# Optimization experiments

Measured on AMD Instinct MI355X. Metric: run time of the kernel, lower is better.

## Reference

```python
import jax, jax.numpy as jnp
import numpy as np

ARITY = 2
DEPTH = 9          # max_depth: full tree has levels 0..DEPTH
H = 512            # hidden_size
V = 512            # vocab_size
B = 64             # batch
S = 64             # source length


def _preorder_perm(arity, depth):
    # map pre-order position -> flat level-order index
    offs = np.cumsum([0] + [arity ** d for d in range(depth + 1)])
    perm = []
    def rec(d, pos):
        perm.append(int(offs[d] + pos))
        if d < depth:
            for c in range(arity):
                rec(d + 1, pos * arity + c)
    rec(0, 0)
    return np.asarray(perm, dtype=np.int32)

PERM = jnp.asarray(_preorder_perm(ARITY, DEPTH))


def setup_inputs() -> dict:
    key = jax.random.key(0)
    ks = jax.random.split(key, 12)
    s = 0.05
    return {
        "root_hiddens": jax.random.normal(ks[0], (B, H), jnp.float32),
        "ann_emb": jax.random.normal(ks[1], (B, H), jnp.float32),
        "encoder_outputs": jax.random.normal(ks[2], (S, B, H), jnp.float32),
        "source_mask": jnp.ones((B, S), dtype=bool),
        # GRUCell params per child: input_size = 2H (attention concat)
        "w_ih": jax.random.normal(ks[3], (ARITY, 3 * H, 2 * H), jnp.float32) * s,
        "w_hh": jax.random.normal(ks[4], (ARITY, 3 * H, H), jnp.float32) * s,
        "b_ih": jax.random.normal(ks[5], (ARITY, 3 * H), jnp.float32) * s,
        "b_hh": jax.random.normal(ks[6], (ARITY, 3 * H), jnp.float32) * s,
        # hidden2vocab: Linear(H,2H) -> Sigmoid -> Linear(2H,V)
        "W1": jax.random.normal(ks[7], (2 * H, H), jnp.float32) * s,
        "b1": jax.random.normal(ks[8], (2 * H,), jnp.float32) * s,
        "W2": jax.random.normal(ks[9], (V, 2 * H), jnp.float32) * s,
        "b2": jax.random.normal(ks[10], (V,), jnp.float32) * s,
    }


def _gru(x, h, wih, whh, bih, bhh):
    # x: [B,n,2H], h: [B,n,H]; PyTorch GRUCell semantics
    gi = jnp.einsum('bni,gi->bng', x, wih) + bih
    gh = jnp.einsum('bnh,gh->bng', h, whh) + bhh
    i_r, i_z, i_n = jnp.split(gi, 3, axis=-1)
    h_r, h_z, h_n = jnp.split(gh, 3, axis=-1)
    r = jax.nn.sigmoid(i_r + h_r)
    z = jax.nn.sigmoid(i_z + h_z)
    n = jnp.tanh(i_n + r * h_n)
    return (1.0 - z) * n + z * h


def _forward(root_hiddens, ann_emb, encoder_outputs, source_mask,
             w_ih, w_hh, b_ih, b_hh, W1, b1, W2, b2):
    b = root_hiddens.shape[0]
    enc = encoder_outputs.transpose(1, 0, 2)        # [B,S,H]
    h = root_hiddens[:, None, :]                    # [B,1,H]
    prods = []
    for d in range(DEPTH + 1):
        # hidden2vocab at every node of this level
        hid = jax.nn.sigmoid(jnp.einsum('bnh,kh->bnk', h, W1) + b1)
        prods.append(jnp.einsum('bnk,vk->bnv', hid, W2) + b2)
        if d < DEPTH:
            # dot-product attention per node over source positions
            scores = jnp.einsum('bnh,bsh->bns', h, enc)
            scores = jnp.where(source_mask[:, None, :], scores, -1e9)
            a = jax.nn.softmax(scores, axis=-1)
            weighted = jnp.einsum('bns,bsh->bnh', a, enc)
            n = h.shape[1]
            x = jnp.concatenate(
                [jnp.broadcast_to(ann_emb[:, None, :], (b, n, H)), weighted],
                axis=-1)                             # [B,n,2H]
            children = [_gru(x, h, w_ih[c], w_hh[c], b_ih[c], b_hh[c])
                        for c in range(ARITY)]
            h = jnp.stack(children, axis=2).reshape(b, n * ARITY, H)
    out = jnp.concatenate(prods, axis=1)            # [B,N,V] level-order
    out = out[:, PERM, :]                           # pre-order, as torch yields
    return out.transpose(1, 0, 2)                   # [N,B,V] like pad_sequence


def reference(root_hiddens, ann_emb, encoder_outputs, source_mask,
              w_ih, w_hh, b_ih, b_hh, W1, b1, W2, b2):
    return _forward(root_hiddens, ann_emb, encoder_outputs, source_mask,
                    w_ih, w_hh, b_ih, b_hh, W1, b1, W2, b2)
```

## Files before the change

kernel.cpp:

```cpp
#include <hip/hip_runtime.h>


#define BATCH 64
#define HDIM  512

typedef float  floatx4 __attribute__((ext_vector_type(4)));
typedef float  f32x16  __attribute__((ext_vector_type(16)));
typedef short  short8  __attribute__((ext_vector_type(8)));

__device__ __forceinline__ float bf2f(unsigned short u) {
  union { unsigned int i; float f; } v; v.i = ((unsigned int)u) << 16; return v.f;
}
__device__ __forceinline__ unsigned short f2bf(float f) {
  union { float f; unsigned int i; } v; v.f = f;
  unsigned int x = v.i;
  return (unsigned short)((x + 0x7fffu + ((x >> 16) & 1u)) >> 16);
}
__device__ __forceinline__ float sigm(float x) { return 1.f / (1.f + __expf(-x)); }

__device__ __forceinline__ int preorder_idx(int d, int node) {
  int p = 0;
  for (int i = 1; i <= d; ++i) {
    int bit = (node >> (d - i)) & 1;
    p += 1 + bit * ((1 << (10 - i)) - 1);
  }
  return p;
}

__device__ __forceinline__ void gload_lds16(const void* g, void* l) {
  __builtin_amdgcn_global_load_lds(
      (const __attribute__((address_space(1))) unsigned int*)g,
      (__attribute__((address_space(3))) unsigned int*)l, 16, 0, 0);
}

__device__ __forceinline__ void stage_f32(unsigned short* ldst, const float* src) {
  float4 v0 = *(const float4*)src;
  float4 v1 = *(const float4*)(src + 4);
  union { unsigned short s[8]; float4 v; } u;
  u.s[0]=f2bf(v0.x); u.s[1]=f2bf(v0.y); u.s[2]=f2bf(v0.z); u.s[3]=f2bf(v0.w);
  u.s[4]=f2bf(v1.x); u.s[5]=f2bf(v1.y); u.s[6]=f2bf(v1.z); u.s[7]=f2bf(v1.w);
  *(float4*)ldst = u.v;
}

__device__ __forceinline__ void stage_split(unsigned short* dh, unsigned short* dl,
                                            const float* src) {
  float4 v0 = *(const float4*)src;
  float4 v1 = *(const float4*)(src + 4);
  float v[8] = {v0.x, v0.y, v0.z, v0.w, v1.x, v1.y, v1.z, v1.w};
  union { unsigned short s[8]; float4 q; } H, L;
  #pragma unroll
  for (int i = 0; i < 8; ++i) {
    unsigned short hb = f2bf(v[i]);
    H.s[i] = hb;
    L.s[i] = f2bf(v[i] - bf2f(hb));
  }
  *(float4*)dh = H.q;
  *(float4*)dl = L.q;
}

__global__ __launch_bounds__(256) void k_root(const float* __restrict__ root,
                                              float* __restrict__ h0,
                                              unsigned short* __restrict__ bh,
                                              unsigned short* __restrict__ bl) {
  int i = blockIdx.x * 256 + threadIdx.x;
  float v = root[i];
  h0[i] = v;
  int row = i >> 9, k = i & 511;
  int mt = row >> 5, r = row & 31, ktg = k >> 4, oct = (k >> 3) & 1, e = k & 7;
  size_t fo = ((size_t)(mt * 32 + ktg) * 64 + oct * 32 + r) * 8 + e;
  unsigned short hb = f2bf(v);
  bh[fo] = hb;
  bl[fo] = f2bf(v - bf2f(hb));
}

__global__ __launch_bounds__(256) void k_prep_wih(const float* __restrict__ wih,
                                                  unsigned short* __restrict__ dh,
                                                  unsigned short* __restrict__ dl) {
  int idx = blockIdx.x * 256 + threadIdx.x;
  int jr  = idx & 31;
  int oct = (idx >> 5) & 1;
  int ktg = (idx >> 6) & 31;
  int jt  = (idx >> 11) & 15;
  int cg  = idx >> 15;
  int c = cg / 3, g = cg % 3;
  int j = jt * 32 + jr, k = ktg * 16 + oct * 8;
  const float* src = wih + ((size_t)c * 1536 + g * 512 + j) * 1024 + 512 + k;
  float v[8];
  *(float4*)&v[0] = *(const float4*)src;
  *(float4*)&v[4] = *(const float4*)(src + 4);
  union { unsigned short s[8]; float4 q; } H, L;
  #pragma unroll
  for (int i = 0; i < 8; ++i) {
    unsigned short hb = f2bf(v[i]); H.s[i] = hb; L.s[i] = f2bf(v[i] - bf2f(hb));
  }
  *(float4*)(dh + (size_t)idx * 8) = H.q;
  *(float4*)(dl + (size_t)idx * 8) = L.q;
}

__global__ __launch_bounds__(256) void k_prep_whh(const float* __restrict__ whh,
                                                  unsigned short* __restrict__ dh,
                                                  unsigned short* __restrict__ dl) {
  int idx = blockIdx.x * 256 + threadIdx.x;
  int jr  = idx & 31;
  int oct = (idx >> 5) & 1;
  int ktg = (idx >> 6) & 31;
  int jt  = (idx >> 11) & 15;
  int cg  = idx >> 15;
  int c = cg / 3, g = cg % 3;
  int j = jt * 32 + jr, k = ktg * 16 + oct * 8;
  const float* src = whh + ((size_t)c * 1536 + g * 512 + j) * 512 + k;
  float v[8];
  *(float4*)&v[0] = *(const float4*)src;
  *(float4*)&v[4] = *(const float4*)(src + 4);
  union { unsigned short s[8]; float4 q; } H, L;
  #pragma unroll
  for (int i = 0; i < 8; ++i) {
    unsigned short hb = f2bf(v[i]); H.s[i] = hb; L.s[i] = f2bf(v[i] - bf2f(hb));
  }
  *(float4*)(dh + (size_t)idx * 8) = H.q;
  *(float4*)(dl + (size_t)idx * 8) = L.q;
}

__global__ __launch_bounds__(256) void k_prep_bf(const float* __restrict__ src,
                                                 unsigned short* __restrict__ db) {
  size_t i = ((size_t)blockIdx.x * 256 + threadIdx.x) * 8;
  stage_f32(db + i, src + i);
}

__global__ __launch_bounds__(256) void k_giann(const float* __restrict__ ann,
                                               const float* __restrict__ wih,
                                               float* __restrict__ giann) {
  __shared__ __align__(16) unsigned short lah[64*40], lal[64*40];
  __shared__ __align__(16) unsigned short lwh[64*40], lwl[64*40];
  int t = threadIdx.x, lane = t & 63, wv = t >> 6;
  int jbase = blockIdx.y * 64, c = blockIdx.z;
  const float* wih_c = wih + (size_t)c * 1536 * 1024;
  floatx4 acc[4];
  #pragma unroll
  for (int i = 0; i < 4; ++i) acc[i] = (floatx4)(0.f);
  int srow = t >> 2, skk = (t & 3) * 8;
  for (int k0 = 0; k0 < 512; k0 += 32) {
    stage_split(lah + srow*40 + skk, lal + srow*40 + skk,
                ann + (size_t)srow * 512 + k0 + skk);
    stage_split(lwh + srow*40 + skk, lwl + srow*40 + skk,
                wih_c + (size_t)(jbase + srow) * 1024 + k0 + skk);
    __syncthreads();
    int arow = wv * 16 + (lane & 15), kq = (lane >> 4) * 8;
    short8 ah = *(const short8*)(lah + arow*40 + kq);
    short8 al = *(const short8*)(lal + arow*40 + kq);
    #pragma unroll
    for (int nt = 0; nt < 4; ++nt) {
      int wo = (nt * 16 + (lane & 15)) * 40 + kq;
      short8 wh = *(const short8*)(lwh + wo);
      short8 wl = *(const short8*)(lwl + wo);
      acc[nt] = __builtin_amdgcn_mfma_f32_16x16x32_bf16(ah, wh, acc[nt], 0, 0, 0);
      acc[nt] = __builtin_amdgcn_mfma_f32_16x16x32_bf16(ah, wl, acc[nt], 0, 0, 0);
      acc[nt] = __builtin_amdgcn_mfma_f32_16x16x32_bf16(al, wh, acc[nt], 0, 0, 0);
    }
    __syncthreads();
  }
  int quad = lane >> 4, cl = lane & 15;
  #pragma unroll
  for (int nt = 0; nt < 4; ++nt) {
    int g = jbase + nt * 16 + cl;
    #pragma unroll
    for (int r = 0; r < 4; ++r) {
      int b = wv * 16 + quad * 4 + r;
      giann[((size_t)c * 64 + b) * 1536 + g] = acc[nt][r];
    }
  }
}

__global__ __launch_bounds__(256) void k_attn(const float* __restrict__ h,
                                              const float* __restrict__ enc,
                                              unsigned short* __restrict__ wgh,
                                              unsigned short* __restrict__ wgl,
                                              int d) {
  int lane = threadIdx.x & 63, wv = threadIdx.x >> 6;
  int m = blockIdx.x * 4 + wv;
  int b = m >> d;
  __shared__ __align__(16) float sh[4][512];
  {
    const float4* src = (const float4*)(h + (size_t)m * HDIM);
    float4* dst = (float4*)sh[wv];
    dst[lane] = src[lane];
    dst[lane + 64] = src[lane + 64];
  }
  __syncthreads();
  const float* hr = sh[wv];
  const float* er = enc + ((size_t)lane * BATCH + b) * HDIM;
  float sc = 0.f;
  for (int k = 0; k < HDIM; k += 8) {
    float4 w0 = *(const float4*)(er + k);
    float4 w1 = *(const float4*)(er + k + 4);
    sc += hr[k+0]*w0.x + hr[k+1]*w0.y + hr[k+2]*w0.z + hr[k+3]*w0.w;
    sc += hr[k+4]*w1.x + hr[k+5]*w1.y + hr[k+6]*w1.z + hr[k+7]*w1.w;
  }
  float mx = sc;
  #pragma unroll
  for (int off = 32; off; off >>= 1) mx = fmaxf(mx, __shfl_xor(mx, off));
  float e = __expf(sc - mx);
  float sum = e;
  #pragma unroll
  for (int off = 32; off; off >>= 1) sum += __shfl_xor(sum, off);
  float a = e / sum;
  float acc[8];
  #pragma unroll
  for (int i = 0; i < 8; ++i) acc[i] = 0.f;
  for (int s = 0; s < 64; ++s) {
    float as = __shfl(a, s);
    const float* ep = enc + ((size_t)s * BATCH + b) * HDIM + lane * 8;
    float4 w0 = *(const float4*)ep;
    float4 w1 = *(const float4*)(ep + 4);
    acc[0] += as * w0.x; acc[1] += as * w0.y; acc[2] += as * w0.z; acc[3] += as * w0.w;
    acc[4] += as * w1.x; acc[5] += as * w1.y; acc[6] += as * w1.z; acc[7] += as * w1.w;
  }
  union { unsigned short s[8]; float4 q; } H, L;
  #pragma unroll
  for (int i = 0; i < 8; ++i) {
    unsigned short hb = f2bf(acc[i]); H.s[i] = hb; L.s[i] = f2bf(acc[i] - bf2f(hb));
  }
  int mt = m >> 5, rr = m & 31;
  size_t fo = ((size_t)(mt * 32 + (lane >> 1)) * 64 + (lane & 1) * 32 + rr) * 8;
  *(float4*)(wgh + fo) = H.q;
  *(float4*)(wgl + fo) = L.q;
}

__global__ __launch_bounds__(256) void k_hid(const float* __restrict__ h,
                                             const unsigned short* __restrict__ W1b,
                                             const float* __restrict__ b1,
                                             unsigned short* __restrict__ hid) {
  __shared__ __align__(16) unsigned short la[64 * 40];
  __shared__ __align__(16) unsigned short lw[64 * 40];
  int t = threadIdx.x, lane = t & 63, wv = t >> 6;
  int mbase = blockIdx.x * 64, jbase = blockIdx.y * 64;
  floatx4 acc[4];
  #pragma unroll
  for (int i = 0; i < 4; ++i) acc[i] = (floatx4)(0.f);
  int srow = t >> 2, skk = (t & 3) * 8;
  for (int k0 = 0; k0 < 512; k0 += 32) {
    stage_f32(la + srow * 40 + skk, h + (size_t)(mbase + srow) * 512 + k0 + skk);
    *(float4*)(lw + srow * 40 + skk) =
        *(const float4*)(W1b + (size_t)(jbase + srow) * 512 + k0 + skk);
    __syncthreads();
    int arow = wv * 16 + (lane & 15);
    int kq = (lane >> 4) * 8;
    short8 af = *(const short8*)(la + arow * 40 + kq);
    #pragma unroll
    for (int nt = 0; nt < 4; ++nt) {
      short8 wf = *(const short8*)(lw + (nt * 16 + (lane & 15)) * 40 + kq);
      acc[nt] = __builtin_amdgcn_mfma_f32_16x16x32_bf16(af, wf, acc[nt], 0, 0, 0);
    }
    __syncthreads();
  }
  int quad = lane >> 4, cl = lane & 15;
  #pragma unroll
  for (int nt = 0; nt < 4; ++nt) {
    int j = jbase + nt * 16 + cl;
    float bias = b1[j];
    #pragma unroll
    for (int r = 0; r < 4; ++r) {
      int m = mbase + wv * 16 + quad * 4 + r;
      hid[(size_t)m * 1024 + j] = f2bf(sigm(acc[nt][r] + bias));
    }
  }
}

__global__ __launch_bounds__(256) void k_out(const unsigned short* __restrict__ hid,
                                             const unsigned short* __restrict__ W2b,
                                             const float* __restrict__ b2,
                                             float* __restrict__ out, int d) {
  __shared__ __align__(16) unsigned short la[64 * 40];
  __shared__ __align__(16) unsigned short lw[64 * 40];
  int t = threadIdx.x, lane = t & 63, wv = t >> 6;
  int mbase = blockIdx.x * 64, jbase = blockIdx.y * 64;
  floatx4 acc[4];
  #pragma unroll
  for (int i = 0; i < 4; ++i) acc[i] = (floatx4)(0.f);
  int srow = t >> 2, skk = (t & 3) * 8;
  for (int k0 = 0; k0 < 1024; k0 += 32) {
    *(float4*)(la + srow * 40 + skk) =
        *(const float4*)(hid + (size_t)(mbase + srow) * 1024 + k0 + skk);
    *(float4*)(lw + srow * 40 + skk) =
        *(const float4*)(W2b + (size_t)(jbase + srow) * 1024 + k0 + skk);
    __syncthreads();
    int arow = wv * 16 + (lane & 15);
    int kq = (lane >> 4) * 8;
    short8 af = *(const short8*)(la + arow * 40 + kq);
    #pragma unroll
    for (int nt = 0; nt < 4; ++nt) {
      short8 wf = *(const short8*)(lw + (nt * 16 + (lane & 15)) * 40 + kq);
      acc[nt] = __builtin_amdgcn_mfma_f32_16x16x32_bf16(af, wf, acc[nt], 0, 0, 0);
    }
    __syncthreads();
  }
  int quad = lane >> 4, cl = lane & 15;
  int nmask = (1 << d) - 1;
  int pv[4], bv[4];
  #pragma unroll
  for (int r = 0; r < 4; ++r) {
    int m = mbase + wv * 16 + quad * 4 + r;
    bv[r] = m >> d;
    pv[r] = preorder_idx(d, m & nmask);
  }
  #pragma unroll
  for (int nt = 0; nt < 4; ++nt) {
    int j = jbase + nt * 16 + cl;
    float bias = b2[j];
    #pragma unroll
    for (int r = 0; r < 4; ++r) {
      out[((size_t)pv[r] * BATCH + bv[r]) * 512 + j] = acc[nt][r] + bias;
    }
  }
}

#define MF32(a, b, c) __builtin_amdgcn_mfma_f32_32x32x16_bf16(a, b, c, 0, 0, 0)

__global__ __launch_bounds__(256, 2) void k_gru(const float* __restrict__ h,
                                             const unsigned short* __restrict__ wgh,
                                             const unsigned short* __restrict__ wgl,
                                             const unsigned short* __restrict__ hbh,
                                             const unsigned short* __restrict__ hbl,
                                             const unsigned short* __restrict__ wihh,
                                             const unsigned short* __restrict__ wihl,
                                             const unsigned short* __restrict__ whhh,
                                             const unsigned short* __restrict__ whhl,
                                             const float* __restrict__ bih,
                                             const float* __restrict__ bhh,
                                             const float* __restrict__ giann,
                                             float* __restrict__ hnext,
                                             unsigned short* __restrict__ nbh,
                                             unsigned short* __restrict__ nbl,
                                             int d, int M, int emit_bf) {
  __shared__ __align__(16) unsigned short smem[2][20 * 512];
  int t = threadIdx.x, lane = t & 63, wv = t >> 6;
  int wm = wv >> 1, wj = wv & 1;
  int c = blockIdx.z;
  int mbase = blockIdx.x * 128, jbase = blockIdx.y * 64;
  int jt0 = jbase >> 5;
  int mb32 = mbase >> 5;
  int mtcap = (M >> 5) - 1;

  f32x16 a_r[2], a_z[2], a_n[2], a_h[2];
  #pragma unroll
  for (int i = 0; i < 2; ++i) {
    a_r[i] = (f32x16)(0.f); a_z[i] = (f32x16)(0.f);
    a_n[i] = (f32x16)(0.f); a_h[i] = (f32x16)(0.f);
  }

  auto stage = [&](int it2, int buf2) {
    int pht = it2 >> 5, kt = it2 & 31;
    const unsigned short* Ah = pht ? hbh : wgh;
    const unsigned short* Al = pht ? hbl : wgl;
    const unsigned short* Wh = pht ? whhh : wihh;
    const unsigned short* Wl = pht ? whhl : wihl;
    #pragma unroll
    for (int q = 0; q < 5; ++q) {
      int f = wv * 5 + q;
      const unsigned short* src;
      if (f < 8) {
        int mtl = f >> 1;
        int mt = mb32 + mtl; if (mt > mtcap) mt = mtcap;
        const unsigned short* blob = (f & 1) ? Al : Ah;
        src = blob + ((size_t)(mt * 32 + kt) * 64 + lane) * 8;
      } else {
        int u = f - 8;
        int g = u >> 2, jtl = (u >> 1) & 1;
        const unsigned short* blob = (u & 1) ? Wl : Wh;
        src = blob + ((size_t)(((c * 3 + g) * 16 + jt0 + jtl) * 32 + kt) * 64
                      + lane) * 8;
      }
      gload_lds16(src, &smem[buf2][f * 512]);
    }
  };

  stage(0, 0);
  __syncthreads();
  #pragma unroll
  for (int ph = 0; ph < 2; ++ph) {
    for (int i = 0; i < 32; ++i) {
      int it = ph * 32 + i;
      int buf = it & 1;
      if (it < 63) stage(it + 1, buf ^ 1);
      const unsigned short* bb = smem[buf];
      short8 ah[2], al[2];
      #pragma unroll
      for (int mt = 0; mt < 2; ++mt) {
        int s = (wm * 2 + mt) * 2;
        ah[mt] = *(const short8*)(bb + s * 512 + lane * 8);
        al[mt] = *(const short8*)(bb + (s + 1) * 512 + lane * 8);
      }
      short8 w[3][2];
      #pragma unroll
      for (int g = 0; g < 3; ++g) {
        int s = 8 + (g * 2 + wj) * 2;
        w[g][0] = *(const short8*)(bb + s * 512 + lane * 8);
        w[g][1] = *(const short8*)(bb + (s + 1) * 512 + lane * 8);
      }
      f32x16* ax = ph ? a_h : a_n;
      #pragma unroll
      for (int mt = 0; mt < 2; ++mt) {
        short8 AH = ah[mt], AL = al[mt];
        a_r[mt] = MF32(AH, w[0][0], a_r[mt]);
        a_r[mt] = MF32(AH, w[0][1], a_r[mt]);
        a_r[mt] = MF32(AL, w[0][0], a_r[mt]);
        a_z[mt] = MF32(AH, w[1][0], a_z[mt]);
        a_z[mt] = MF32(AH, w[1][1], a_z[mt]);
        a_z[mt] = MF32(AL, w[1][0], a_z[mt]);
        ax[mt]  = MF32(AH, w[2][0], ax[mt]);
        ax[mt]  = MF32(AH, w[2][1], ax[mt]);
        ax[mt]  = MF32(AL, w[2][0], ax[mt]);
      }
      __syncthreads();
    }
  }

  unsigned short (*trh)[72] = (unsigned short(*)[72])(&smem[0][0]);
  unsigned short (*trl)[72] = (unsigned short(*)[72])(&smem[0][0] + 128 * 72);
  int cl = lane & 31;
  int j = jbase + wj * 32 + cl;
  float br  = bih[c * 1536 + j]        + bhh[c * 1536 + j];
  float bz  = bih[c * 1536 + 512 + j]  + bhh[c * 1536 + 512 + j];
  float bin = bih[c * 1536 + 1024 + j];
  float bhn = bhh[c * 1536 + 1024 + j];
  int rowoff = 4 * (lane >> 5);
  #pragma unroll
  for (int mt = 0; mt < 2; ++mt) {
    int mb0 = mbase + wm * 64 + mt * 32 + rowoff;
    #pragma unroll
    for (int r = 0; r < 16; ++r) {
      int m = mb0 + (r & 3) + 8 * (r >> 2);
      if (m < M) {
        int b = m >> d;
        const float* gp = giann + ((size_t)c * 64 + b) * 1536 + j;
        float rg = sigm(a_r[mt][r] + gp[0] + br);
        float zg = sigm(a_z[mt][r] + gp[512] + bz);
        float ng = tanhf(a_n[mt][r] + gp[1024] + bin + rg * (a_h[mt][r] + bhn));
        float hv = h[(size_t)m * 512 + j];
        float nh = (1.f - zg) * ng + zg * hv;
        hnext[(size_t)(2 * m + c) * 512 + j] = nh;
        if (emit_bf) {
          unsigned short hb = f2bf(nh);
          trh[m - mbase][j - jbase] = hb;
          trl[m - mbase][j - jbase] = f2bf(nh - bf2f(hb));
        }
      }
    }
  }
  if (emit_bf) {
    __syncthreads();
    int a = t >> 7;
    int row = t & 127;
    if (mbase + row < M) {
      const unsigned short* trp = a ? &trl[row][0] : &trh[row][0];
      unsigned short* dst = a ? nbl : nbh;
      int mp = 2 * (mbase + row) + c;
      int mtp = mp >> 5, rp = mp & 31;
      #pragma unroll
      for (int q = 0; q < 8; ++q) {
        int k = jbase + q * 8;
        int ktg = k >> 4, oct = (k >> 3) & 1;
        float4 v = *(const float4*)(trp + q * 8);
        *(float4*)(dst + ((size_t)(mtp * 32 + ktg) * 64 + oct * 32 + rp) * 8) = v;
      }
    }
  }
}

extern "C" void kernel_launch(void* const* d_in, const int* in_sizes, int n_in,
                              void* d_out, int out_size, void* d_ws, size_t ws_size,
                              hipStream_t stream) {
  const float* root = (const float*)d_in[0];
  const float* ann  = (const float*)d_in[1];
  const float* enc  = (const float*)d_in[2];
  const float* wih  = (const float*)d_in[4];
  const float* whh  = (const float*)d_in[5];
  const float* bih  = (const float*)d_in[6];
  const float* bhh  = (const float*)d_in[7];
  const float* W1   = (const float*)d_in[8];
  const float* b1   = (const float*)d_in[9];
  const float* W2   = (const float*)d_in[10];
  const float* b2   = (const float*)d_in[11];
  float* out = (float*)d_out;

  char* ws = (char*)d_ws;
  float* hA = (float*)ws;
  float* hB = (float*)(ws + (size_t)67108864);
  unsigned short* hid  = (unsigned short*)(ws + (size_t)100663296);
  unsigned short* wgh  = (unsigned short*)(ws + (size_t)134217728);
  unsigned short* wgl  = (unsigned short*)(ws + (size_t)150994944);
  unsigned short* hbEh = (unsigned short*)(ws + (size_t)167772160);
  unsigned short* hbEl = (unsigned short*)(ws + (size_t)184549376);
  unsigned short* hbOh = (unsigned short*)(ws + (size_t)201326592);
  unsigned short* hbOl = (unsigned short*)(ws + (size_t)209715200);
  float* giann         = (float*)(ws + (size_t)218103808);
  unsigned short* wihh = (unsigned short*)(ws + (size_t)218890240);
  unsigned short* wihl = (unsigned short*)(ws + (size_t)222035968);
  unsigned short* whhh = (unsigned short*)(ws + (size_t)225181696);
  unsigned short* whhl = (unsigned short*)(ws + (size_t)228327424);
  unsigned short* W1b  = (unsigned short*)(ws + (size_t)231473152);
  unsigned short* W2b  = (unsigned short*)(ws + (size_t)232521728);

  k_root<<<dim3(128), dim3(256), 0, stream>>>(root, hB, hbEh, hbEl);
  k_prep_wih<<<dim3(768), dim3(256), 0, stream>>>(wih, wihh, wihl);
  k_prep_whh<<<dim3(768), dim3(256), 0, stream>>>(whh, whhh, whhl);
  k_prep_bf<<<dim3(256), dim3(256), 0, stream>>>(W1, W1b);
  k_prep_bf<<<dim3(256), dim3(256), 0, stream>>>(W2, W2b);
  k_giann<<<dim3(1, 24, 2), dim3(256), 0, stream>>>(ann, wih, giann);

  float* hcur = hB;
  float* hnxt = hA;
  unsigned short *bhc = hbEh, *blc = hbEl, *bhn = hbOh, *bln = hbOl;
  for (int d = 0; d <= 9; ++d) {
    int n = 1 << d;
    int M = 64 * n;
    k_hid<<<dim3(M / 64, 16), dim3(256), 0, stream>>>(hcur, W1b, b1, hid);
    k_out<<<dim3(M / 64, 8), dim3(256), 0, stream>>>(hid, W2b, b2, out, d);
    if (d < 9) {
      k_attn<<<dim3(M / 4), dim3(256), 0, stream>>>(hcur, enc, wgh, wgl, d);
      k_gru<<<dim3((M + 127) / 128, 8, 2), dim3(256), 0, stream>>>(
          hcur, wgh, wgl, bhc, blc, wihh, wihl, whhh, whhl, bih, bhh, giann,
          hnxt, bhn, bln, d, M, d < 8 ? 1 : 0);
      float* tmp = hcur; hcur = hnxt; hnxt = tmp;
      unsigned short* ts;
      ts = bhc; bhc = bhn; bhn = ts;
      ts = blc; blc = bln; bln = ts;
    }
  }
}
```

Baseline: 2.419 ms.

## Triple-buffer GRU GEMM LDS staging with explicit vmcnt waits and barriers

Replaces the double-buffered LDS pipeline in the GRU kernel with a three-stage ring buffer. Two tiles are now prefetched ahead, and partial s_waitcnt vmcnt counts let global-to-LDS loads stay in flight across iterations instead of draining at every __syncthreads. It also raises wave priority around the MFMA block. The cost is 50% more shared memory, which may reduce occupancy at 2 blocks/CU, and the hand-tuned wait counts depend on the exact number of loads per stage.

```diff
diff --git a/kernel.cpp b/kernel.cpp
--- a/kernel.cpp
+++ b/kernel.cpp
@@ -332,7 +332,7 @@
                                              unsigned short* __restrict__ nbh,
                                              unsigned short* __restrict__ nbl,
                                              int d, int M, int emit_bf) {
-  __shared__ __align__(16) unsigned short smem[2][20 * 512];
+  __shared__ __align__(16) unsigned short smem[3][20 * 512];
   int t = threadIdx.x, lane = t & 63, wv = t >> 6;
   int wm = wv >> 1, wj = wv & 1;
   int c = blockIdx.z;
@@ -375,13 +375,18 @@
   };
 
   stage(0, 0);
-  __syncthreads();
+  stage(1, 1);
+  stage(2, 2);
+  asm volatile("s_waitcnt vmcnt(10)" ::: "memory");
+  __builtin_amdgcn_s_barrier();
+  __builtin_amdgcn_sched_barrier(0);
+
+  int buf = 0;
   #pragma unroll
   for (int ph = 0; ph < 2; ++ph) {
-    for (int i = 0; i < 32; ++i) {
-      int it = ph * 32 + i;
-      int buf = it & 1;
-      if (it < 63) stage(it + 1, buf ^ 1);
+    f32x16* axr = ph ? a_h : a_n;
+    for (int i2 = 0; i2 < 32; ++i2) {
+      int it = ph * 32 + i2;
       const unsigned short* bb = smem[buf];
       short8 ah[2], al[2];
       #pragma unroll
@@ -397,7 +402,12 @@
         w[g][0] = *(const short8*)(bb + s * 512 + lane * 8);
         w[g][1] = *(const short8*)(bb + (s + 1) * 512 + lane * 8);
       }
-      f32x16* ax = ph ? a_h : a_n;
+      asm volatile("s_waitcnt lgkmcnt(0)" ::: "memory");
+      __builtin_amdgcn_sched_barrier(0);
+      __builtin_amdgcn_s_barrier();
+      __builtin_amdgcn_sched_barrier(0);
+      if (it + 3 < 64) stage(it + 3, buf);
+      __builtin_amdgcn_s_setprio(1);
       #pragma unroll
       for (int mt = 0; mt < 2; ++mt) {
         short8 AH = ah[mt], AL = al[mt];
@@ -407,11 +417,23 @@
         a_z[mt] = MF32(AH, w[1][0], a_z[mt]);
         a_z[mt] = MF32(AH, w[1][1], a_z[mt]);
         a_z[mt] = MF32(AL, w[1][0], a_z[mt]);
-        ax[mt]  = MF32(AH, w[2][0], ax[mt]);
-        ax[mt]  = MF32(AH, w[2][1], ax[mt]);
-        ax[mt]  = MF32(AL, w[2][0], ax[mt]);
-      }
-      __syncthreads();
+        axr[mt] = MF32(AH, w[2][0], axr[mt]);
+        axr[mt] = MF32(AH, w[2][1], axr[mt]);
+        axr[mt] = MF32(AL, w[2][0], axr[mt]);
+      }
+      __builtin_amdgcn_s_setprio(0);
+      __builtin_amdgcn_sched_barrier(0);
+      if (it < 61) {
+        asm volatile("s_waitcnt vmcnt(10)" ::: "memory");
+      } else if (it == 61) {
+        asm volatile("s_waitcnt vmcnt(5)" ::: "memory");
+      } else {
+        asm volatile("s_waitcnt vmcnt(0)" ::: "memory");
+      }
+      __builtin_amdgcn_sched_barrier(0);
+      __builtin_amdgcn_s_barrier();
+      __builtin_amdgcn_sched_barrier(0);
+      buf = (buf == 2) ? 0 : buf + 1;
     }
   }
 
```

Measured after the change: 2.334 ms. -3.5%, faster.
